# Performance work log

Measured on AMD Instinct MI355X. Metric: run time of the kernel, lower is better.

Reference implementation:

```python
import jax, jax.numpy as jnp
import numpy as np

B, S, HID = 2, 2048, 4096
NH, NKV, HD = 32, 8, 128
SLIDING_WINDOW = 1024
ROPE_THETA = 10000.0


def setup_inputs() -> dict:
    key = jax.random.key(0)
    ks = jax.random.split(key, 6)
    hidden_states = jax.random.normal(ks[0], (B, S, HID), dtype=jnp.float32)
    attention_mask = jnp.ones((B, S), dtype=jnp.int32)
    position_ids = jnp.broadcast_to(jnp.arange(S, dtype=jnp.int32)[None, :], (B, S))
    sc = 1.0 / np.sqrt(HID)
    q_w = jax.random.normal(ks[1], (HID, NH * HD), dtype=jnp.float32) * sc
    k_w = jax.random.normal(ks[2], (HID, NKV * HD), dtype=jnp.float32) * sc
    v_w = jax.random.normal(ks[3], (HID, NKV * HD), dtype=jnp.float32) * sc
    o_w = jax.random.normal(ks[4], (NH * HD, HID), dtype=jnp.float32) * sc
    return {"hidden_states": hidden_states, "attention_mask": attention_mask,
            "position_ids": position_ids, "q_w": q_w, "k_w": k_w, "v_w": v_w, "o_w": o_w}


def _rotate_half(x):
    return jnp.concatenate((-x[..., x.shape[-1] // 2:], x[..., : x.shape[-1] // 2]), axis=-1)


def _rope_sincos(position_ids):
    # inv_freq over even dims of head_dim; emb = concat(freqs, freqs)
    inv_freq = 1.0 / ROPE_THETA ** (jnp.arange(0, HD, 2, dtype=jnp.float32) / HD)
    freqs = position_ids.astype(jnp.float32)[..., None] * inv_freq  # [B,S,HD/2]
    emb = jnp.concatenate((freqs, freqs), axis=-1)                  # [B,S,HD]
    # broadcast over heads axis: [B,S,1,HD]
    return jnp.sin(emb)[:, :, None, :], jnp.cos(emb)[:, :, None, :]


def reference(hidden_states, attention_mask, position_ids, q_w, k_w, v_w, o_w):
    b, q_len, _ = hidden_states.shape
    n_rep = NH // NKV

    q = (hidden_states @ q_w).reshape(b, q_len, NH, HD)
    k = (hidden_states @ k_w).reshape(b, q_len, NKV, HD)
    v = (hidden_states @ v_w).reshape(b, q_len, NKV, HD)

    sin_pos, cos_pos = _rope_sincos(position_ids)
    q = q * cos_pos + _rotate_half(q) * sin_pos
    k = k * cos_pos + _rotate_half(k) * sin_pos

    # GQA: repeat kv heads (repeat_interleave along head axis)
    k = jnp.repeat(k, n_rep, axis=2)  # [B,S,NH,HD]
    v = jnp.repeat(v, n_rep, axis=2)

    # sliding-window causal mask: j <= i and j >= i - sliding_window
    i = jnp.arange(q_len)[:, None]
    j = jnp.arange(q_len)[None, :]
    band = (j <= i) & (j >= i - SLIDING_WINDOW)           # [Q,K]
    mask = band[None, None] & (attention_mask[:, None, None, :] > 0)  # [B,1,Q,K]

    bias = jnp.where(mask, 0.0, jnp.finfo(jnp.float32).min)

    scale = 1.0 / jnp.sqrt(jnp.asarray(HD, dtype=jnp.float32))
    scores = jnp.einsum('bqhd,bkhd->bhqk', q, k) * scale + bias
    attn_weights = jax.nn.softmax(scores, axis=-1)
    attn_out = jnp.einsum('bhqk,bkhd->bqhd', attn_weights, v)
    attn_out = attn_out.reshape(b, q_len, HID)
    return attn_out @ o_w
```

## Files before the change

kernel.cpp:

```cpp
#include <hip/hip_runtime.h>
#include <stdint.h>
#include <stddef.h>

typedef __bf16 bf16x8 __attribute__((ext_vector_type(8)));
typedef short short8 __attribute__((ext_vector_type(8)));
typedef float floatx4 __attribute__((ext_vector_type(4)));
typedef unsigned short ushort4v __attribute__((ext_vector_type(4)));

#define LOG2E 1.44269504088896340736f
#define SM_SCALE 0.08838834764831845f

__device__ __forceinline__ unsigned short f2bf(float f){
  unsigned int u = __float_as_uint(f);
  u += 0x7fffu + ((u >> 16) & 1u);
  return (unsigned short)(u >> 16);
}
__device__ __forceinline__ float bf2f(unsigned short s){
  return __uint_as_float(((unsigned int)s) << 16);
}
__device__ __forceinline__ void gl2lds16(const void* g, void* l){
  __builtin_amdgcn_global_load_lds((const __attribute__((address_space(1))) void*)g,
                                   (__attribute__((address_space(3))) void*)l, 16, 0, 0);
}

__global__ __launch_bounds__(256) void conv_f32_bf16(const float* __restrict__ in,
                                                     unsigned short* __restrict__ out){
  int t = blockIdx.x * 256 + threadIdx.x;
  floatx4 v = *(const floatx4*)(in + (size_t)t * 4);
  ushort4v o;
#pragma unroll
  for (int j = 0; j < 4; ++j) o[j] = f2bf(v[j]);
  *(ushort4v*)(out + (size_t)t * 4) = o;
}

__global__ __launch_bounds__(256) void transpose_cvt(const float* __restrict__ in,
                                                     unsigned short* __restrict__ out,
                                                     int Kd, int Nd){
  __shared__ __align__(16) unsigned short tile[64 * 80];
  int n0 = blockIdx.x * 64, k0 = blockIdx.y * 64;
  int t = threadIdx.x;
#pragma unroll
  for (int it = 0; it < 2; ++it){
    int rr = (t >> 3) + it * 32;
    int cc = t & 7;
    const float* src = in + (size_t)(k0 + rr) * Nd + n0 + cc * 8;
    floatx4 a = *(const floatx4*)src;
    floatx4 b = *(const floatx4*)(src + 4);
    short8 s;
#pragma unroll
    for (int j = 0; j < 4; ++j){ s[j] = (short)f2bf(a[j]); s[j + 4] = (short)f2bf(b[j]); }
    *(short8*)&tile[rr * 80 + cc * 8] = s;
  }
  __syncthreads();
#pragma unroll
  for (int it = 0; it < 2; ++it){
    int nr = (t >> 3) + it * 32;
    int kc = t & 7;
    short8 v;
#pragma unroll
    for (int j = 0; j < 8; ++j) v[j] = (short)tile[(kc * 8 + j) * 80 + nr];
    *(short8*)(out + (size_t)(n0 + nr) * Kd + k0 + kc * 8) = v;
  }
}

__global__ __launch_bounds__(256, 2) void gemm_bt(
    const unsigned short* __restrict__ A,
    const unsigned short* __restrict__ Wq,
    const unsigned short* __restrict__ Wk,
    const unsigned short* __restrict__ Wv,
    unsigned short* __restrict__ oQ,
    unsigned short* __restrict__ oK,
    unsigned short* __restrict__ oVt,
    float* __restrict__ oF, int f32out)
{
  __shared__ __align__(16) unsigned short As[128 * 64];
  __shared__ __align__(16) unsigned short Bs[128 * 64];
  const int tid = threadIdx.x;
  const int w = tid >> 6, lane = tid & 63, quad = lane >> 4, l15 = lane & 15;
  const int wm64 = (w >> 1) * 64, wn64 = (w & 1) * 64;
  const int m0 = blockIdx.y * 128;
  const int n0 = blockIdx.x * 128;

  const unsigned short* Wsrc;
  int nb, region;
  if (n0 < 4096)      { Wsrc = Wq; nb = n0;        region = 0; }
  else if (n0 < 5120) { Wsrc = Wk; nb = n0 - 4096; region = 1; }
  else                { Wsrc = Wv; nb = n0 - 5120; region = 2; }

  floatx4 acc[4][4];
#pragma unroll
  for (int i = 0; i < 4; ++i)
#pragma unroll
    for (int j = 0; j < 4; ++j) acc[i][j] = (floatx4){0.f, 0.f, 0.f, 0.f};

  const int rsub = lane >> 3, csub = lane & 7;

  for (int k0 = 0; k0 < 4096; k0 += 64){
#pragma unroll
    for (int i = 0; i < 4; ++i){
      int u = i * 4 + w;
      int r = u * 8 + rsub;
      gl2lds16(A    + ((size_t)(m0 + r) << 12) + k0 + ((csub ^ (r & 7)) << 3), (char*)As + u * 1024);
      gl2lds16(Wsrc + ((size_t)(nb + r) << 12) + k0 + ((csub ^ (r & 7)) << 3), (char*)Bs + u * 1024);
    }
    __syncthreads();
#pragma unroll
    for (int ks = 0; ks < 2; ++ks){
      bf16x8 af[4], bfr[4];
#pragma unroll
      for (int mt = 0; mt < 4; ++mt){
        int r = wm64 + mt * 16 + l15;
        int kc = ks * 4 + quad;
        af[mt] = *(const bf16x8*)&As[r * 64 + ((kc ^ (r & 7)) << 3)];
      }
#pragma unroll
      for (int nt = 0; nt < 4; ++nt){
        int r = wn64 + nt * 16 + l15;
        int kc = ks * 4 + quad;
        bfr[nt] = *(const bf16x8*)&Bs[r * 64 + ((kc ^ (r & 7)) << 3)];
      }
#pragma unroll
      for (int mt = 0; mt < 4; ++mt)
#pragma unroll
        for (int nt = 0; nt < 4; ++nt)
          acc[mt][nt] = __builtin_amdgcn_mfma_f32_16x16x32_bf16(af[mt], bfr[nt], acc[mt][nt], 0, 0, 0);
    }
    __syncthreads();
  }

  if (region == 0){
    if (f32out){
#pragma unroll
      for (int mt = 0; mt < 4; ++mt)
#pragma unroll
        for (int nt = 0; nt < 4; ++nt){
          int gn = n0 + wn64 + nt * 16 + l15;
#pragma unroll
          for (int rr = 0; rr < 4; ++rr){
            int gm = m0 + wm64 + mt * 16 + quad * 4 + rr;
            oF[((size_t)gm << 12) + gn] = acc[mt][nt][rr];
          }
        }
    } else {
#pragma unroll
      for (int mt = 0; mt < 4; ++mt)
#pragma unroll
        for (int nt = 0; nt < 4; ++nt){
          int gn = n0 + wn64 + nt * 16 + l15;
#pragma unroll
          for (int rr = 0; rr < 4; ++rr){
            int gm = m0 + wm64 + mt * 16 + quad * 4 + rr;
            oQ[((size_t)gm << 12) + gn] = f2bf(acc[mt][nt][rr]);
          }
        }
    }
  } else if (region == 1){
#pragma unroll
    for (int mt = 0; mt < 4; ++mt)
#pragma unroll
      for (int nt = 0; nt < 4; ++nt){
        int gn = n0 - 4096 + wn64 + nt * 16 + l15;
#pragma unroll
        for (int rr = 0; rr < 4; ++rr){
          int gm = m0 + wm64 + mt * 16 + quad * 4 + rr;
          oK[((size_t)gm << 10) + gn] = f2bf(acc[mt][nt][rr]);
        }
      }
  } else {
#pragma unroll
    for (int mt = 0; mt < 4; ++mt){
      int gm0 = m0 + wm64 + mt * 16 + quad * 4;
      int b = gm0 >> 11, s0 = gm0 & 2047;
#pragma unroll
      for (int nt = 0; nt < 4; ++nt){
        int dg = n0 - 5120 + wn64 + nt * 16 + l15;
        int kvh = dg >> 7, d = dg & 127;
        ushort4v pk;
#pragma unroll
        for (int rr = 0; rr < 4; ++rr) pk[rr] = f2bf(acc[mt][nt][rr]);
        *(ushort4v*)(oVt + (((size_t)(b * 8 + kvh) * 128 + d) * 2048 + s0)) = pk;
      }
    }
  }
}

__global__ void rope_apply_k(unsigned short* __restrict__ Qb, unsigned short* __restrict__ Kb,
                             const int* __restrict__ pos){
  int t = blockIdx.x * 256 + threadIdx.x;
  unsigned short* base;
  int row, ch;
  if (t < 1048576){ row = t >> 8; int c = t & 255; base = Qb + ((size_t)row << 12) + (c >> 3) * 128; ch = c & 7; }
  else { int t2 = t - 1048576; row = t2 >> 6; int c = t2 & 63; base = Kb + ((size_t)row << 10) + (c >> 3) * 128; ch = c & 7; }
  float p = (float)pos[row];
  int d0 = ch * 8;
  short8 x0 = *(short8*)(base + d0);
  short8 x1 = *(short8*)(base + d0 + 64);
  short8 y0, y1;
#pragma unroll
  for (int j = 0; j < 8; ++j){
    float ang = p * exp2f(-(float)(d0 + j) * 0.20762050593045952f);
    float sn = sinf(ang), cs = cosf(ang);
    float a  = bf2f((unsigned short)x0[j]);
    float bb = bf2f((unsigned short)x1[j]);
    y0[j] = (short)f2bf(a * cs - bb * sn);
    y1[j] = (short)f2bf(bb * cs + a * sn);
  }
  *(short8*)(base + d0)      = y0;
  *(short8*)(base + d0 + 64) = y1;
}

__global__ __launch_bounds__(256, 2) void flash_swa(
    const unsigned short* __restrict__ Q,
    const unsigned short* __restrict__ K,
    const unsigned short* __restrict__ Vt,
    const int* __restrict__ amask,
    unsigned short* __restrict__ attn)
{
  __shared__ __align__(16) unsigned short Kl[64 * 128];
  __shared__ __align__(16) unsigned short Vl[128 * 64];
  __shared__ __align__(16) unsigned short Pl[4 * 16 * 88];
  const int qt = blockIdx.x, h = blockIdx.y, b = blockIdx.z;
  const int kv = h >> 2;
  const int tid = threadIdx.x, w = tid >> 6, lane = tid & 63, quad = lane >> 4, l15 = lane & 15;
  const int q0 = qt * 64;

  bf16x8 qf[4];
  {
    const unsigned short* qbase = Q + (((size_t)(b * 2048 + q0 + w * 16 + l15)) << 12) + h * 128;
#pragma unroll
    for (int ks = 0; ks < 4; ++ks) qf[ks] = *(const bf16x8*)(qbase + ks * 32 + quad * 8);
  }
  floatx4 acco[8];
#pragma unroll
  for (int i = 0; i < 8; ++i) acco[i] = (floatx4){0.f, 0.f, 0.f, 0.f};
  float m_i[4] = {-1e30f, -1e30f, -1e30f, -1e30f};
  float l_i[4] = {0.f, 0.f, 0.f, 0.f};

  const int ts = (qt >= 16) ? (qt - 16) : 0;
  for (int jt = ts; jt <= qt; ++jt){
    const int k0 = jt * 64;
#pragma unroll
    for (int i = 0; i < 4; ++i){
      int u = i * 4 + w;
      int r = u * 4 + (lane >> 4);
      int c = lane & 15;
      gl2lds16(K + (((size_t)(b * 2048 + k0 + r)) << 10) + kv * 128 + ((c ^ (r & 15)) << 3),
               (char*)Kl + u * 1024);
    }
#pragma unroll
    for (int i = 0; i < 4; ++i){
      int u = i * 4 + w;
      int d = u * 8 + (lane >> 3);
      int c = lane & 7;
      gl2lds16(Vt + ((size_t)(b * 8 + kv) * 128 + d) * 2048 + k0 + ((c ^ (d & 7)) << 3),
               (char*)Vl + u * 1024);
    }
    __syncthreads();

    floatx4 accs[4];
#pragma unroll
    for (int i = 0; i < 4; ++i) accs[i] = (floatx4){0.f, 0.f, 0.f, 0.f};
#pragma unroll
    for (int ks = 0; ks < 4; ++ks)
#pragma unroll
      for (int nt = 0; nt < 4; ++nt){
        int r = nt * 16 + l15;
        int kc = ks * 4 + quad;
        bf16x8 kf = *(const bf16x8*)&Kl[r * 128 + ((kc ^ (r & 15)) << 3)];
        accs[nt] = __builtin_amdgcn_mfma_f32_16x16x32_bf16(qf[ks], kf, accs[nt], 0, 0, 0);
      }

#pragma unroll
    for (int nt = 0; nt < 4; ++nt){
      int j = k0 + nt * 16 + l15;
      int mk = amask[b * 2048 + j];
#pragma unroll
      for (int rr = 0; rr < 4; ++rr){
        int irow = q0 + w * 16 + quad * 4 + rr;
        bool valid = (j <= irow) && (j >= irow - 1024) && (mk > 0);
        accs[nt][rr] = valid ? accs[nt][rr] * SM_SCALE : -1e30f;
      }
    }
    float alpha[4];
#pragma unroll
    for (int rr = 0; rr < 4; ++rr){
      float v = fmaxf(fmaxf(accs[0][rr], accs[1][rr]), fmaxf(accs[2][rr], accs[3][rr]));
#pragma unroll
      for (int d_ = 1; d_ < 16; d_ <<= 1) v = fmaxf(v, __shfl_xor(v, d_));
      float mnew = fmaxf(m_i[rr], v);
      alpha[rr] = exp2f((m_i[rr] - mnew) * LOG2E);
      m_i[rr] = mnew;
      float rs = 0.f;
#pragma unroll
      for (int nt = 0; nt < 4; ++nt){
        float p = exp2f((accs[nt][rr] - mnew) * LOG2E);
        accs[nt][rr] = p;
        rs += p;
      }
#pragma unroll
      for (int d_ = 1; d_ < 16; d_ <<= 1) rs += __shfl_xor(rs, d_);
      l_i[rr] = l_i[rr] * alpha[rr] + rs;
    }
#pragma unroll
    for (int nt = 0; nt < 4; ++nt)
#pragma unroll
      for (int rr = 0; rr < 4; ++rr)
        Pl[w * 1408 + (quad * 4 + rr) * 88 + nt * 16 + l15] = f2bf(accs[nt][rr]);
#pragma unroll
    for (int n2 = 0; n2 < 8; ++n2)
#pragma unroll
      for (int rr = 0; rr < 4; ++rr)
        acco[n2][rr] *= alpha[rr];
#pragma unroll
    for (int ks2 = 0; ks2 < 2; ++ks2){
      bf16x8 pf = *(const bf16x8*)&Pl[w * 1408 + l15 * 88 + ks2 * 32 + quad * 8];
#pragma unroll
      for (int n2 = 0; n2 < 8; ++n2){
        int d = n2 * 16 + l15;
        int sc = ks2 * 4 + quad;
        bf16x8 vf = *(const bf16x8*)&Vl[d * 64 + ((sc ^ (d & 7)) << 3)];
        acco[n2] = __builtin_amdgcn_mfma_f32_16x16x32_bf16(pf, vf, acco[n2], 0, 0, 0);
      }
    }
    __syncthreads();
  }

  float inv[4];
#pragma unroll
  for (int rr = 0; rr < 4; ++rr) inv[rr] = 1.f / l_i[rr];
#pragma unroll
  for (int n2 = 0; n2 < 8; ++n2)
#pragma unroll
    for (int rr = 0; rr < 4; ++rr){
      size_t off = (((size_t)(b * 2048 + q0 + w * 16 + quad * 4 + rr)) << 12) + h * 128 + n2 * 16 + l15;
      attn[off] = f2bf(acco[n2][rr] * inv[rr]);
    }
}

extern "C" void kernel_launch(void* const* d_in, const int* in_sizes, int n_in,
                              void* d_out, int out_size, void* d_ws, size_t ws_size,
                              hipStream_t stream){
  const float* hidden = (const float*)d_in[0];
  const int* amask = (const int*)d_in[1];
  const int* pos   = (const int*)d_in[2];
  const float* qw = (const float*)d_in[3];
  const float* kw = (const float*)d_in[4];
  const float* vw = (const float*)d_in[5];
  const float* ow = (const float*)d_in[6];

  char* ws = (char*)d_ws;
  unsigned short* hb   = (unsigned short*)(ws + 0);
  unsigned short* qt   = (unsigned short*)(ws + 33554432);
  unsigned short* kt   = (unsigned short*)(ws + 67108864);
  unsigned short* vtw  = (unsigned short*)(ws + 75497472);
  unsigned short* Qb   = (unsigned short*)(ws + 83886080);
  unsigned short* Kb   = (unsigned short*)(ws + 117440512);
  unsigned short* Vtb  = (unsigned short*)(ws + 125829120);
  unsigned short* ot   = hb;
  unsigned short* attn = qt;
  float* outp = (float*)d_out;

  hipLaunchKernelGGL(conv_f32_bf16, dim3(16384), dim3(256), 0, stream, hidden, hb);
  hipLaunchKernelGGL(transpose_cvt, dim3(64, 64), dim3(256), 0, stream, qw, qt, 4096, 4096);
  hipLaunchKernelGGL(transpose_cvt, dim3(16, 64), dim3(256), 0, stream, kw, kt, 4096, 1024);
  hipLaunchKernelGGL(transpose_cvt, dim3(16, 64), dim3(256), 0, stream, vw, vtw, 4096, 1024);
  hipLaunchKernelGGL(gemm_bt, dim3(48, 32), dim3(256), 0, stream,
                     hb, qt, kt, vtw, Qb, Kb, Vtb, (float*)nullptr, 0);
  hipLaunchKernelGGL(transpose_cvt, dim3(64, 64), dim3(256), 0, stream, ow, ot, 4096, 4096);
  hipLaunchKernelGGL(rope_apply_k, dim3(5120), dim3(256), 0, stream, Qb, Kb, pos);
  hipLaunchKernelGGL(flash_swa, dim3(32, 32, 2), dim3(256), 0, stream, Qb, Kb, Vtb, amask, attn);
  hipLaunchKernelGGL(gemm_bt, dim3(32, 32), dim3(256), 0, stream,
                     attn, ot, ot, ot, nullptr, nullptr, nullptr, outp, 1);
}
```

Baseline: 794.2 us.

## Fold softmax scale into Q, skip interior masking, lazy rescale, swizzle P LDS

Folds the softmax scale and log2e factor into Q during the RoPE pass, so the flash kernel uses raw exp2 without per-element multiplies. The mask is applied only on diagonal and window-edge tiles, or when the attention mask has zeros, which the kernel detects with a wave ballot. Output rescaling happens lazily, only when the running max grows by more than a threshold. The padded P buffer becomes an XOR-swizzled layout, and launch bounds now target 4 blocks per CU, which may pressure registers. Lazy rescaling keeps accumulators bounded but relies on the threshold to avoid overflow.

```diff
diff --git a/kernel.cpp b/kernel.cpp
--- a/kernel.cpp
+++ b/kernel.cpp
@@ -6,9 +6,6 @@
 typedef short short8 __attribute__((ext_vector_type(8)));
 typedef float floatx4 __attribute__((ext_vector_type(4)));
 typedef unsigned short ushort4v __attribute__((ext_vector_type(4)));
-
-#define LOG2E 1.44269504088896340736f
-#define SM_SCALE 0.08838834764831845f
 
 __device__ __forceinline__ unsigned short f2bf(float f){
   unsigned int u = __float_as_uint(f);
@@ -189,9 +186,12 @@
   int t = blockIdx.x * 256 + threadIdx.x;
   unsigned short* base;
   int row, ch;
-  if (t < 1048576){ row = t >> 8; int c = t & 255; base = Qb + ((size_t)row << 12) + (c >> 3) * 128; ch = c & 7; }
+  bool isq = (t < 1048576);
+  if (isq){ row = t >> 8; int c = t & 255; base = Qb + ((size_t)row << 12) + (c >> 3) * 128; ch = c & 7; }
   else { int t2 = t - 1048576; row = t2 >> 6; int c = t2 & 63; base = Kb + ((size_t)row << 10) + (c >> 3) * 128; ch = c & 7; }
   float p = (float)pos[row];
+  const float qs = 0.08838834764831845f * 1.44269504088896340736f;
+  float sc_out = isq ? qs : 1.0f;
   int d0 = ch * 8;
   short8 x0 = *(short8*)(base + d0);
   short8 x1 = *(short8*)(base + d0 + 64);
@@ -202,14 +202,14 @@
     float sn = sinf(ang), cs = cosf(ang);
     float a  = bf2f((unsigned short)x0[j]);
     float bb = bf2f((unsigned short)x1[j]);
-    y0[j] = (short)f2bf(a * cs - bb * sn);
-    y1[j] = (short)f2bf(bb * cs + a * sn);
+    y0[j] = (short)f2bf((a * cs - bb * sn) * sc_out);
+    y1[j] = (short)f2bf((bb * cs + a * sn) * sc_out);
   }
   *(short8*)(base + d0)      = y0;
   *(short8*)(base + d0 + 64) = y1;
 }
 
-__global__ __launch_bounds__(256, 2) void flash_swa(
+__global__ __launch_bounds__(256, 4) void flash_swa(
     const unsigned short* __restrict__ Q,
     const unsigned short* __restrict__ K,
     const unsigned short* __restrict__ Vt,
@@ -218,7 +218,7 @@
 {
   __shared__ __align__(16) unsigned short Kl[64 * 128];
   __shared__ __align__(16) unsigned short Vl[128 * 64];
-  __shared__ __align__(16) unsigned short Pl[4 * 16 * 88];
+  __shared__ __align__(16) unsigned short Pl[4 * 16 * 64];
   const int qt = blockIdx.x, h = blockIdx.y, b = blockIdx.z;
   const int kv = h >> 2;
   const int tid = threadIdx.x, w = tid >> 6, lane = tid & 63, quad = lane >> 4, l15 = lane & 15;
@@ -255,6 +255,8 @@
       gl2lds16(Vt + ((size_t)(b * 8 + kv) * 128 + d) * 2048 + k0 + ((c ^ (d & 7)) << 3),
                (char*)Vl + u * 1024);
     }
+    int mkl = amask[b * 2048 + k0 + lane];
+    bool allv = (__ballot(mkl > 0) == ~0ull);
     __syncthreads();
 
     floatx4 accs[4];
@@ -270,50 +272,64 @@
         accs[nt] = __builtin_amdgcn_mfma_f32_16x16x32_bf16(qf[ks], kf, accs[nt], 0, 0, 0);
       }
 
-#pragma unroll
-    for (int nt = 0; nt < 4; ++nt){
-      int j = k0 + nt * 16 + l15;
-      int mk = amask[b * 2048 + j];
-#pragma unroll
-      for (int rr = 0; rr < 4; ++rr){
-        int irow = q0 + w * 16 + quad * 4 + rr;
-        bool valid = (j <= irow) && (j >= irow - 1024) && (mk > 0);
-        accs[nt][rr] = valid ? accs[nt][rr] * SM_SCALE : -1e30f;
-      }
-    }
-    float alpha[4];
+    bool slow = (jt == qt) || ((qt - jt) == 16) || (!allv);
+    if (slow){
+#pragma unroll
+      for (int nt = 0; nt < 4; ++nt){
+        int j = k0 + nt * 16 + l15;
+        int mk = amask[b * 2048 + j];
+#pragma unroll
+        for (int rr = 0; rr < 4; ++rr){
+          int irow = q0 + w * 16 + quad * 4 + rr;
+          bool valid = (j <= irow) && (j >= irow - 1024) && (mk > 0);
+          accs[nt][rr] = valid ? accs[nt][rr] : -1e30f;
+        }
+      }
+    }
+
+    float vmax[4]; float need = 0.f;
 #pragma unroll
     for (int rr = 0; rr < 4; ++rr){
       float v = fmaxf(fmaxf(accs[0][rr], accs[1][rr]), fmaxf(accs[2][rr], accs[3][rr]));
 #pragma unroll
       for (int d_ = 1; d_ < 16; d_ <<= 1) v = fmaxf(v, __shfl_xor(v, d_));
-      float mnew = fmaxf(m_i[rr], v);
-      alpha[rr] = exp2f((m_i[rr] - mnew) * LOG2E);
-      m_i[rr] = mnew;
+      vmax[rr] = v;
+      need = fmaxf(need, v - m_i[rr]);
+    }
+    if (!__all(need <= 8.0f)){
+#pragma unroll
+      for (int rr = 0; rr < 4; ++rr){
+        float mnew = fmaxf(m_i[rr], vmax[rr]);
+        float alpha = exp2f(m_i[rr] - mnew);
+        m_i[rr] = mnew;
+        l_i[rr] *= alpha;
+#pragma unroll
+        for (int n2 = 0; n2 < 8; ++n2) acco[n2][rr] *= alpha;
+      }
+    }
+#pragma unroll
+    for (int rr = 0; rr < 4; ++rr){
       float rs = 0.f;
 #pragma unroll
       for (int nt = 0; nt < 4; ++nt){
-        float p = exp2f((accs[nt][rr] - mnew) * LOG2E);
+        float p = exp2f(accs[nt][rr] - m_i[rr]);
         accs[nt][rr] = p;
         rs += p;
       }
 #pragma unroll
       for (int d_ = 1; d_ < 16; d_ <<= 1) rs += __shfl_xor(rs, d_);
-      l_i[rr] = l_i[rr] * alpha[rr] + rs;
+      l_i[rr] += rs;
     }
 #pragma unroll
     for (int nt = 0; nt < 4; ++nt)
 #pragma unroll
-      for (int rr = 0; rr < 4; ++rr)
-        Pl[w * 1408 + (quad * 4 + rr) * 88 + nt * 16 + l15] = f2bf(accs[nt][rr]);
-#pragma unroll
-    for (int n2 = 0; n2 < 8; ++n2)
-#pragma unroll
-      for (int rr = 0; rr < 4; ++rr)
-        acco[n2][rr] *= alpha[rr];
+      for (int rr = 0; rr < 4; ++rr){
+        int row = quad * 4 + rr;
+        Pl[w * 1024 + row * 64 + ((nt * 16 + l15) ^ ((row & 7) << 3))] = f2bf(accs[nt][rr]);
+      }
 #pragma unroll
     for (int ks2 = 0; ks2 < 2; ++ks2){
-      bf16x8 pf = *(const bf16x8*)&Pl[w * 1408 + l15 * 88 + ks2 * 32 + quad * 8];
+      bf16x8 pf = *(const bf16x8*)&Pl[w * 1024 + l15 * 64 + ((ks2 * 32 + quad * 8) ^ ((l15 & 7) << 3))];
 #pragma unroll
       for (int n2 = 0; n2 < 8; ++n2){
         int d = n2 * 16 + l15;
```

New measurement: 774.4 us. 1.03x faster.
